# Optimization experiments

Hardware: AMD Instinct MI355X
Metric: run time of the kernel (lower is better)

Reference implementation:

```python
import jax, jax.numpy as jnp
import numpy as np

EPS = 1e-4

def _conv(x, W):
    # x: [B,H,W,Cin], W: [3,3,Cin,Cout] -> SAME submanifold-style dense conv
    return jax.lax.conv_general_dilated(x, W, (1, 1), 'SAME',
                                        dimension_numbers=('NHWC', 'HWIO', 'NHWC'))

def _bn_relu(x, m, g, b):
    # BatchNormReLU over active sites only (scn semantics)
    mm = m[..., None]
    n = jnp.maximum(mm.sum(), 1.0)
    mean = (x * mm).sum((0, 1, 2)) / n
    var = (((x - mean) ** 2) * mm).sum((0, 1, 2)) / n
    y = (x - mean) * jax.lax.rsqrt(var + EPS) * g + b
    return jnp.maximum(y, 0.0) * mm

def _maxpool(x, m):
    # scn.MaxPooling(2, 3, 2): 3x3 window, stride 2, VALID; output active if any input active
    neg = jnp.where(m[..., None] > 0, x, -1e30)
    p = jax.lax.reduce_window(neg, -1e30, jax.lax.max, (1, 3, 3, 1), (1, 2, 2, 1), 'VALID')
    m2 = jax.lax.reduce_window(m, 0.0, jax.lax.max, (1, 3, 3), (1, 2, 2), 'VALID')
    return jnp.where(m2[..., None] > 0, p, 0.0), m2


def setup_inputs() -> dict:
    key = jax.random.key(0)
    ks = jax.random.split(key, 16)
    B, H, W = 2048, 23, 31
    x = jax.random.normal(ks[0], (B, H, W, 2), dtype=jnp.float32)
    mask = jax.random.randint(ks[1], (B, H, W), 0, 2, dtype=jnp.int32)
    def w(k, shape, s=0.05):
        return jax.random.normal(k, shape, dtype=jnp.float32) * s
    params = {
        'x': x, 'mask': mask,
        'W1': w(ks[2], (3, 3, 2, 16)),   'g1': jnp.ones(16),  'b1': jnp.zeros(16),
        'W2': w(ks[3], (3, 3, 16, 32)),  'g2': jnp.ones(32),  'b2': jnp.zeros(32),
        'W3': w(ks[4], (3, 3, 32, 64)),  'g3': jnp.ones(64),  'b3': jnp.zeros(64),
        'W4': w(ks[5], (3, 3, 64, 128)), 'g4': jnp.ones(128), 'b4': jnp.zeros(128),
        'Wl': w(ks[6], (3, 3, 128, 4 * 256)), 'bl': jnp.zeros(4 * 256),
        'lw1': w(ks[7], (8960, 1024), 0.02), 'lb1': jnp.zeros(1024),
        'lw2': w(ks[8], (1024, 5 * 7 * 12), 0.02), 'lb2': jnp.zeros(5 * 7 * 12),
    }
    return params


def reference(x, mask, W1, g1, b1, W2, g2, b2, W3, g3, b3, W4, g4, b4,
              Wl, bl, lw1, lb1, lw2, lb2):
    m = mask.astype(x.dtype)
    xm = x * m[..., None]
    h = _bn_relu(_conv(xm, W1) * m[..., None], m, g1, b1)
    h = _bn_relu(_conv(h, W2) * m[..., None], m, g2, b2)
    h, m = _maxpool(h, m)                          # [B,11,15,32]
    h = _bn_relu(_conv(h, W3) * m[..., None], m, g3, b3)
    h = _bn_relu(_conv(h, W4) * m[..., None], m, g4, b4)
    h, m = _maxpool(h, m)                          # [B,5,7,128]
    # sparse ConvLSTM, single step, zero initial hidden/cell state
    gates = (_conv(h, Wl) + bl) * m[..., None]     # [B,5,7,1024]
    i, f, o, g_ = jnp.split(gates, 4, axis=-1)
    c = jax.nn.sigmoid(i) * jnp.tanh(g_)
    hh = jax.nn.sigmoid(o) * jnp.tanh(c) * m[..., None]  # [B,5,7,256]
    # SparseToDense gives [B,C,H,W]; flatten in (C,H,W) order like torch .view
    flat = jnp.transpose(hh, (0, 3, 1, 2)).reshape(hh.shape[0], -1)  # [B,8960]
    y = jnp.maximum(flat @ lw1 + lb1, 0.0)
    y = y @ lw2 + lb2
    return y.reshape(-1, 5, 7, 12)
```

## Files before the change

### kernel.cpp

```cpp
#include <hip/hip_runtime.h>
#include <hip/hip_bf16.h>
#include <math.h>

using bf16 = __hip_bfloat16;

typedef short s8v __attribute__((ext_vector_type(8)));
typedef float f4v __attribute__((ext_vector_type(4)));

static constexpr int  BB  = 2048;
static constexpr int  IH  = 23, IW = 31;
static constexpr int  PH  = 11, PW = 15;
static constexpr int  QH  = 5,  QW = 7;
static constexpr long NSITE1 = (long)BB * IH * IW;
static constexpr long NSITE2 = (long)BB * PH * PW;
static constexpr long NSITE3 = (long)BB * QH * QW;

static constexpr long OFF_S1 = 0,   OFF_Q1 = 64;
static constexpr long OFF_S2 = 128, OFF_Q2 = 192;
static constexpr long OFF_S3 = 256, OFF_Q3 = 320;
static constexpr long OFF_S4 = 384, OFF_Q4 = 512;
static constexpr long OFF_N1 = 640, OFF_N2 = 641;
static constexpr long OFF_SC1 = 704,  OFF_SH1 = 768;
static constexpr long OFF_SC2 = 832,  OFF_SH2 = 896;
static constexpr long OFF_SC3 = 960,  OFF_SH3 = 1024;
static constexpr long OFF_SC4 = 1088, OFF_SH4 = 1216;
static constexpr long OFF_M0 = 2048;
static constexpr long OFF_M1 = OFF_M0 + NSITE1;
static constexpr long OFF_M2 = OFF_M1 + NSITE2;
static constexpr long OFF_BF = 1871872;
static constexpr long SZ_A   = 43253760L;
static constexpr long WB2_A  = 25000000L;
static constexpr long WB3_B  = 22000000L;
static constexpr long WB4_B  = 22100000L;
static constexpr long WBL_A  = 20000000L;
static constexpr long WFC1_B = 23000000L;
static constexpr long WFC2_B = 33000000L;

__device__ __forceinline__ float b2f(bf16 v) { return __bfloat162float(v); }
__device__ __forceinline__ bf16  f2b(float v) { return __float2bfloat16(v); }
__device__ __forceinline__ float sigmoidf_(float x) {
    return __builtin_amdgcn_rcpf(1.f + __expf(-x));
}
__device__ __forceinline__ float tanhf_(float x) {
    float xc = fminf(fmaxf(x, -15.f), 15.f);
    float t = __expf(-2.f * xc);
    return (1.f - t) * __builtin_amdgcn_rcpf(1.f + t);
}

__device__ __forceinline__ void ld8(const bf16* p, float* f) {
    union { uint4 u; unsigned short s[8]; } cv;
    cv.u = *(const uint4*)p;
#pragma unroll
    for (int i = 0; i < 8; i++) f[i] = __uint_as_float(((unsigned int)cv.s[i]) << 16);
}
__device__ __forceinline__ void st8(bf16* p, const float* f) {
    union { uint4 u; bf16 h[8]; } cv;
#pragma unroll
    for (int i = 0; i < 8; i++) cv.h[i] = f2b(f[i]);
    *(uint4*)p = cv.u;
}

__global__ void cvt_w_k(const float* __restrict__ W, bf16* __restrict__ wb,
                        int CIN, int CINP, int COUT, int total) {
    int idx = blockIdx.x * 256 + threadIdx.x;
    if (idx >= total) return;
    int ci  = idx % CINP;
    int t2  = idx / CINP;
    int co  = t2 % COUT;
    int tap = t2 / COUT;
    wb[idx] = (ci < CIN) ? f2b(W[((long)(tap * CIN + ci)) * COUT + co]) : f2b(0.f);
}

__global__ void cvt_wl3_k(const float* __restrict__ Wl, bf16* __restrict__ wbl3) {
    int idx = blockIdx.x * 256 + threadIdx.x;
    if (idx >= 884736) return;
    int kidx = idx & 31;
    int n    = (idx >> 5) % 768;
    int kk   = (idx >> 5) / 768 % 4;
    int tap  = idx / (32 * 768 * 4);
    int g = n >> 8, c = n & 255;
    int col = (g == 0) ? c : (g == 1 ? 512 + c : 768 + c);
    int cin = kk * 32 + kidx;
    wbl3[idx] = f2b(Wl[((long)(tap * 128 + cin)) * 1024 + col]);
}

__global__ void cvt_fc1T8_k(const float* __restrict__ lw1, bf16* __restrict__ wfc1) {
    int t = blockIdx.x * 256 + threadIdx.x;
    if (t >= 1146880) return;
    int j   = t & 1023;
    int k8g = t >> 10;
    int hw  = k8g >> 5;
    int c8  = k8g & 31;
    float f[8];
#pragma unroll
    for (int c7 = 0; c7 < 8; c7++)
        f[c7] = lw1[((long)((c8 * 8 + c7) * 35 + hw)) * 1024 + j];
    st8(wfc1 + (long)t * 8, f);
}

__global__ void cvt_fc2T8_k(const float* __restrict__ lw2, bf16* __restrict__ whi,
                            bf16* __restrict__ wlo) {
    int t = blockIdx.x * 256 + threadIdx.x;
    if (t >= 57344) return;
    int n  = t % 448;
    int k8 = t / 448;
    union { uint4 u; bf16 h8[8]; } h, l;
#pragma unroll
    for (int ki = 0; ki < 8; ki++) {
        float v = (n < 420) ? lw2[(long)(k8 * 8 + ki) * 420 + n] : 0.f;
        bf16 hb = f2b(v);
        h.h8[ki] = hb;
        l.h8[ki] = f2b(v - b2f(hb));
    }
    *(uint4*)(whi + (long)t * 8) = h.u;
    *(uint4*)(wlo + (long)t * 8) = l.u;
}

__global__ void prep_k(const float* __restrict__ x, const int* __restrict__ mask,
                       float* __restrict__ m0, bf16* __restrict__ xm) {
    long idx = (long)blockIdx.x * 256 + threadIdx.x;
    if (idx >= NSITE1) return;
    float m = (mask[idx] != 0) ? 1.f : 0.f;
    m0[idx] = m;
    xm[idx * 2 + 0] = f2b(x[idx * 2 + 0] * m);
    xm[idx * 2 + 1] = f2b(x[idx * 2 + 1] * m);
}

__global__ void conv1_k(const bf16* __restrict__ xm, const float* __restrict__ Wt,
                        const float* __restrict__ m0, bf16* __restrict__ out) {
    const int H = IH, W = IW;
    long site = (long)blockIdx.x * 256 + threadIdx.x;
    if (site >= NSITE1) return;
    float acc[16];
#pragma unroll
    for (int i = 0; i < 16; i++) acc[i] = 0.f;
    float mk = m0[site];
    if (mk > 0.f) {
        int w = (int)(site % W); int h = (int)((site / W) % H);
        for (int tap = 0; tap < 9; tap++) {
            int dh = tap / 3 - 1, dw = tap % 3 - 1;
            int nh = h + dh, nw = w + dw;
            if (nh < 0 || nh >= H || nw < 0 || nw >= W) continue;
            long ns = site + (long)dh * W + dw;
            float i0 = b2f(xm[ns * 2 + 0]), i1 = b2f(xm[ns * 2 + 1]);
            const float* wp = Wt + tap * 32;
#pragma unroll
            for (int co = 0; co < 16; co++) acc[co] += i0 * wp[co] + i1 * wp[16 + co];
        }
    }
    st8(out + site * 16, acc);
    st8(out + site * 16 + 8, acc + 8);
}

template<int CIN, int CINP, int COUT, int KK, int MT_W, int NT_W, int H, int W, bool ZPAD, bool BN>
__global__ void conv_mfma(const bf16* __restrict__ in, const bf16* __restrict__ wb,
                          const float* __restrict__ mask,
                          const float* __restrict__ scale, const float* __restrict__ shift,
                          bf16* __restrict__ out) {
    constexpr int NT   = COUT / 16;
    constexpr int NWN  = NT / NT_W;
    constexpr int HALO = W + 1;
    constexpr int REG  = 64 + 2 * HALO;
    constexpr int SE   = CIN + 8;
    constexpr int CHPS = CIN / 8;
    __shared__ bf16 smem[(REG + 1) * SE];

    const int tid = threadIdx.x;
    const int wv = tid >> 6;
    const int L  = tid & 63;
    const int q  = (L >> 4);
    const int lm = L & 15;
    const int wn = wv % NWN;
    const int wm = wv / NWN;
    const int mt0 = wm * MT_W;
    const long base = (long)blockIdx.x * 64;
    const long nsites = (long)gridDim.x * 64;

    for (int c = tid; c < REG * CHPS; c += 256) {
        int s = c / CHPS;
        int o = c % CHPS;
        long gs = base - HALO + s;
        uint4 v = {0u, 0u, 0u, 0u};
        if (gs >= 0 && gs < nsites) {
            v = *(const uint4*)(in + gs * CIN + o * 8);
            if (BN) {
                float mk = mask[gs];
                union { uint4 u; unsigned short us[8]; } cv; cv.u = v;
                union { uint4 u; bf16 h[8]; } ov;
#pragma unroll
                for (int i = 0; i < 8; i++) {
                    float f = __uint_as_float(((unsigned int)cv.us[i]) << 16);
                    int ch = o * 8 + i;
                    float r = fmaxf(f * scale[ch] + shift[ch], 0.f);
                    ov.h[i] = f2b(mk > 0.f ? r : 0.f);
                }
                v = ov.u;
            }
        }
        *(uint4*)(smem + s * SE + o * 8) = v;
    }
    if (ZPAD) {
        uint4 z = {0u, 0u, 0u, 0u};
        for (int s = tid; s < REG; s += 256)
            *(uint4*)(smem + s * SE + CIN) = z;
        if (tid == 0)
            *(uint4*)(smem + REG * SE) = z;
    }
    __syncthreads();

    int hh[MT_W], ww[MT_W];
#pragma unroll
    for (int i = 0; i < MT_W; i++) {
        long s = base + (mt0 + i) * 16 + lm;
        ww[i] = (int)(s % W);
        hh[i] = (int)((s / W) % H);
    }
    const int lbase = mt0 * 16 + lm + HALO;

    f4v acc[MT_W][NT_W];
#pragma unroll
    for (int i = 0; i < MT_W; i++)
#pragma unroll
        for (int j = 0; j < NT_W; j++) acc[i][j] = (f4v){0.f, 0.f, 0.f, 0.f};

    for (int tap = 0; tap < 9; tap++) {
        const int dh = tap / 3 - 1, dw = tap % 3 - 1;
        const int dlo = dh * W + dw;
#pragma unroll
        for (int kk = 0; kk < KK; kk++) {
            s8v a[MT_W];
#pragma unroll
            for (int i = 0; i < MT_W; i++) {
                int nh = hh[i] + dh, nw = ww[i] + dw;
                bool ok = (nh >= 0) & (nh < H) & (nw < W) & (nw >= 0);
                s8v t = *(const s8v*)(smem + (lbase + i * 16 + dlo) * SE + kk * 32 + q * 8);
                a[i] = ok ? t : (s8v){0, 0, 0, 0, 0, 0, 0, 0};
            }
#pragma unroll
            for (int j = 0; j < NT_W; j++) {
                int co = (wn * NT_W + j) * 16 + lm;
                s8v b = *(const s8v*)(wb + ((long)(tap * COUT + co)) * CINP + kk * 32 + q * 8);
#pragma unroll
                for (int i = 0; i < MT_W; i++)
                    acc[i][j] = __builtin_amdgcn_mfma_f32_16x16x32_bf16(a[i], b, acc[i][j], 0, 0, 0);
            }
        }
    }
#pragma unroll
    for (int i = 0; i < MT_W; i++) {
#pragma unroll
        for (int r = 0; r < 4; r++) {
            long so = base + (mt0 + i) * 16 + q * 4 + r;
            float mk = mask[so];
#pragma unroll
            for (int j = 0; j < NT_W; j++) {
                int co = (wn * NT_W + j) * 16 + lm;
                out[so * COUT + co] = f2b(mk > 0.f ? acc[i][j][r] : 0.f);
            }
        }
    }
}

template<int C>
__global__ void bn_stats(const bf16* __restrict__ v, const float* __restrict__ mask,
                         float* __restrict__ sum, float* __restrict__ sumsq,
                         float* __restrict__ count, long nsites) {
    __shared__ float s_sum[C], s_ss[C];
    __shared__ float s_cnt;
    int tid = threadIdx.x;
    if (tid < C) { s_sum[tid] = 0.f; s_ss[tid] = 0.f; }
    if (tid == 0) s_cnt = 0.f;
    __syncthreads();
    const long total8 = nsites * C / 8;
    const long stride = (long)gridDim.x * 256;
    const int c0 = (int)((((long)blockIdx.x * 256 + tid) * 8) % C);
    float ls[8], lss[8];
#pragma unroll
    for (int i = 0; i < 8; i++) { ls[i] = 0.f; lss[i] = 0.f; }
    float lc = 0.f;
    for (long e8 = (long)blockIdx.x * 256 + tid; e8 < total8; e8 += stride) {
        long e0 = e8 * 8;
        float f[8];
        ld8(v + e0, f);
#pragma unroll
        for (int i = 0; i < 8; i++) { ls[i] += f[i]; lss[i] += f[i] * f[i]; }
        if (count != nullptr && c0 == 0) lc += (mask[e0 / C] > 0.f) ? 1.f : 0.f;
    }
#pragma unroll
    for (int i = 0; i < 8; i++) {
        atomicAdd(&s_sum[c0 + i], ls[i]);
        atomicAdd(&s_ss[c0 + i], lss[i]);
    }
    if (count != nullptr && c0 == 0) atomicAdd(&s_cnt, lc);
    __syncthreads();
    if (tid < C) { atomicAdd(&sum[tid], s_sum[tid]); atomicAdd(&sumsq[tid], s_ss[tid]); }
    if (count != nullptr && tid == 0) atomicAdd(count, s_cnt);
}

template<int C>
__global__ void bn_param(const float* __restrict__ sum, const float* __restrict__ ss,
                         const float* __restrict__ count,
                         const float* __restrict__ g, const float* __restrict__ b,
                         float* __restrict__ scale, float* __restrict__ shift) {
    int c = threadIdx.x;
    if (c >= C) return;
    float n = fmaxf(count[0], 1.f);
    float mean = sum[c] / n;
    float var  = ss[c] / n - mean * mean;
    float sc = (1.f / sqrtf(var + 1e-4f)) * g[c];
    scale[c] = sc;
    shift[c] = b[c] - mean * sc;
}

template<int C>
__global__ void maxpool_bn(const bf16* __restrict__ in, const float* __restrict__ min_,
                           const float* __restrict__ scale, const float* __restrict__ shift,
                           bf16* __restrict__ out, float* __restrict__ mout,
                           int B, int H, int W, int OH, int OW) {
    long i8 = (long)blockIdx.x * 256 + threadIdx.x;
    long total8 = (long)B * OH * OW * C / 8;
    if (i8 >= total8) return;
    long e0 = i8 * 8;
    int c0 = (int)(e0 % C);
    long osite = e0 / C;
    int ow = (int)(osite % OW); long t2 = osite / OW; int oh = (int)(t2 % OH); long b = t2 / OH;
    float sc[8], sh[8];
#pragma unroll
    for (int i = 0; i < 8; i++) { sc[i] = scale[c0 + i]; sh[i] = shift[c0 + i]; }
    float mm = 0.f, p[8];
#pragma unroll
    for (int i = 0; i < 8; i++) p[i] = -1e30f;
    for (int kh = 0; kh < 3; kh++)
    for (int kw = 0; kw < 3; kw++) {
        int h = oh * 2 + kh, w = ow * 2 + kw;
        long is = ((long)b * H + h) * W + w;
        float mv = min_[is];
        if (mv > 0.f) {
            mm = 1.f;
            float f[8];
            ld8(in + is * C + c0, f);
#pragma unroll
            for (int i = 0; i < 8; i++) p[i] = fmaxf(p[i], f[i] * sc[i] + sh[i]);
        }
    }
    float o[8];
#pragma unroll
    for (int i = 0; i < 8; i++) o[i] = (mm > 0.f) ? fmaxf(p[i], 0.f) : 0.f;
    st8(out + e0, o);
    if (c0 == 0) mout[osite] = mm;
}

__global__ void maxpool_p2t(const bf16* __restrict__ c4, const float* __restrict__ m1,
                            const float* __restrict__ scale, const float* __restrict__ shift,
                            bf16* __restrict__ p2T8, float* __restrict__ m2h) {
    int t = blockIdx.x * 256 + threadIdx.x;
    if (t >= 1146880) return;
    int b  = t & 2047;
    int q2 = t >> 11;
    int hw = q2 % 35;
    int k8 = q2 / 35;
    int oh = hw / QW, ow = hw % QW;
    int c0 = k8 * 8;
    float sc[8], sh[8];
#pragma unroll
    for (int i = 0; i < 8; i++) { sc[i] = scale[c0 + i]; sh[i] = shift[c0 + i]; }
    float mm = 0.f, p[8];
#pragma unroll
    for (int i = 0; i < 8; i++) p[i] = -1e30f;
    for (int kh = 0; kh < 3; kh++)
    for (int kw = 0; kw < 3; kw++) {
        int h = oh * 2 + kh, w = ow * 2 + kw;
        long is = ((long)b * PH + h) * PW + w;
        float mv = m1[is];
        if (mv > 0.f) {
            mm = 1.f;
            float f[8];
            ld8(c4 + is * 128 + c0, f);
#pragma unroll
            for (int i = 0; i < 8; i++) p[i] = fmaxf(p[i], f[i] * sc[i] + sh[i]);
        }
    }
    float o[8];
#pragma unroll
    for (int i = 0; i < 8; i++) o[i] = (mm > 0.f) ? fmaxf(p[i], 0.f) : 0.f;
    st8(p2T8 + (long)t * 8, o);
    if (k8 == 0) m2h[hw * 2048 + b] = mm;
}

__global__ void __launch_bounds__(256, 3)
gates_mfma(const bf16* __restrict__ p2T8, const bf16* __restrict__ wbl3,
           const float* __restrict__ bl, const float* __restrict__ m2h,
           bf16* __restrict__ goutT8) {
    __shared__ bf16 abuf[16 * 64 * 8];
    __shared__ bf16 sm[64][136];
    const int bi = blockIdx.x;
    const int half = bi & 1;
    const int g2 = bi >> 1;
    const int hw = g2 >> 5;
    const int b0 = (g2 & 31) * 64;
    const int h = hw / QW, w = hw % QW;
    const int tid = threadIdx.x;
    const int wv = tid >> 6;
    const int L  = tid & 63;
    const int q  = L >> 4;
    const int lm = L & 15;

    f4v acc[4][2][3];
#pragma unroll
    for (int i = 0; i < 4; i++)
#pragma unroll
        for (int j = 0; j < 2; j++)
#pragma unroll
            for (int g = 0; g < 3; g++) acc[i][j][g] = (f4v){0.f, 0.f, 0.f, 0.f};

    for (int tap = 0; tap < 9; tap++) {
        const int dh = tap / 3 - 1, dw = tap % 3 - 1;
        const int nh = h + dh, nw = w + dw;
        if (nh < 0 || nh >= QH || nw < 0 || nw >= QW) continue;
        const int hwn = hw + dh * QW + dw;

        __syncthreads();
        for (int c = tid; c < 1024; c += 256) {
            int kq = c >> 6;
            int bb = c & 63;
            uint4 v = *(const uint4*)(p2T8 + (((long)(kq * 35 + hwn)) * 2048 + b0 + bb) * 8);
            *(uint4*)(abuf + (long)c * 8) = v;
        }
        __syncthreads();

#pragma unroll
        for (int kk = 0; kk < 4; kk++) {
            s8v a[4];
#pragma unroll
            for (int i = 0; i < 4; i++)
                a[i] = *(const s8v*)(abuf + (((kk * 4 + q) * 64) + i * 16 + lm) * 8);
            const bf16* slab = wbl3 + ((long)(tap * 4 + kk)) * 768 * 32 + (long)q * 8;
#pragma unroll
            for (int j = 0; j < 2; j++) {
                int cc = half * 8 + wv * 2 + j;
#pragma unroll
                for (int g = 0; g < 3; g++) {
                    int n = g * 256 + cc * 16 + lm;
                    s8v b = *(const s8v*)(slab + (long)n * 32);
#pragma unroll
                    for (int i = 0; i < 4; i++)
                        acc[i][j][g] = __builtin_amdgcn_mfma_f32_16x16x32_bf16(a[i], b, acc[i][j][g], 0, 0, 0);
                }
            }
        }
    }
#pragma unroll
    for (int j = 0; j < 2; j++) {
        int cc = half * 8 + wv * 2 + j;
        int c = cc * 16 + lm;
        int cl = (wv * 2 + j) * 16 + lm;
        float bi_ = bl[c], bo_ = bl[512 + c], bg_ = bl[768 + c];
#pragma unroll
        for (int i = 0; i < 4; i++) {
#pragma unroll
            for (int r = 0; r < 4; r++) {
                int b_in = i * 16 + q * 4 + r;
                float m = m2h[hw * 2048 + b0 + b_in];
                float val = 0.f;
                if (m > 0.f) {
                    float iv = acc[i][j][0][r] + bi_;
                    float ov = acc[i][j][1][r] + bo_;
                    float gv = acc[i][j][2][r] + bg_;
                    float ct = sigmoidf_(iv) * tanhf_(gv);
                    val = sigmoidf_(ov) * tanhf_(ct);
                }
                sm[b_in][cl] = f2b(val);
            }
        }
    }
    __syncthreads();
#pragma unroll
    for (int k = 0; k < 4; k++) {
        int e = k * 256 + tid;
        int c8l = e >> 6, b_in = e & 63;
        union { uint4 u; bf16 h8[8]; } v;
#pragma unroll
        for (int i = 0; i < 8; i++) v.h8[i] = sm[b_in][c8l * 8 + i];
        long dst = ((long)(hw * 32 + half * 16 + c8l)) * 2048 + b0 + b_in;
        *(uint4*)(goutT8 + dst * 8) = v.u;
    }
}

__global__ void fc1_mfma(const bf16* __restrict__ AT8, const bf16* __restrict__ WT8,
                         const float* __restrict__ lb1, bf16* __restrict__ y1) {
    const int tid = threadIdx.x;
    const int wv = tid >> 6;
    const int L  = tid & 63;
    const int q  = L >> 4, lm = L & 15;
    const int wm = wv >> 1, wn = wv & 1;
    const int bm = blockIdx.x & 31;
    const int bn = blockIdx.x >> 5;
    const int m0 = bm * 64 + wm * 32;
    const int n0 = bn * 64 + wn * 32;

    f4v acc[2][2];
#pragma unroll
    for (int i = 0; i < 2; i++)
#pragma unroll
        for (int j = 0; j < 2; j++) acc[i][j] = (f4v){0.f, 0.f, 0.f, 0.f};

#pragma unroll 2
    for (int k8 = 0; k8 < 1120; k8 += 4) {
        long ar = ((long)(k8 + q)) * 2048;
        long br = ((long)(k8 + q)) * 1024;
        s8v a0 = *(const s8v*)(AT8 + (ar + m0 + lm) * 8);
        s8v a1 = *(const s8v*)(AT8 + (ar + m0 + 16 + lm) * 8);
        s8v b0 = *(const s8v*)(WT8 + (br + n0 + lm) * 8);
        s8v b1 = *(const s8v*)(WT8 + (br + n0 + 16 + lm) * 8);
        acc[0][0] = __builtin_amdgcn_mfma_f32_16x16x32_bf16(a0, b0, acc[0][0], 0, 0, 0);
        acc[0][1] = __builtin_amdgcn_mfma_f32_16x16x32_bf16(a0, b1, acc[0][1], 0, 0, 0);
        acc[1][0] = __builtin_amdgcn_mfma_f32_16x16x32_bf16(a1, b0, acc[1][0], 0, 0, 0);
        acc[1][1] = __builtin_amdgcn_mfma_f32_16x16x32_bf16(a1, b1, acc[1][1], 0, 0, 0);
    }
#pragma unroll
    for (int i = 0; i < 2; i++) {
#pragma unroll
        for (int j = 0; j < 2; j++) {
            int nn = n0 + j * 16 + lm;
            float bias = lb1[nn];
#pragma unroll
            for (int r = 0; r < 4; r++) {
                int mm = m0 + i * 16 + q * 4 + r;
                y1[(long)mm * 1024 + nn] = f2b(fmaxf(acc[i][j][r] + bias, 0.f));
            }
        }
    }
}

__global__ void fc2_mfma(const bf16* __restrict__ y1, const bf16* __restrict__ whi,
                         const bf16* __restrict__ wlo, const float* __restrict__ lb2,
                         float* __restrict__ out) {
    const int tid = threadIdx.x;
    const int wv = tid >> 6;
    const int L  = tid & 63;
    const int q  = L >> 4, lm = L & 15;
    const int wm = wv >> 1, wn = wv & 1;
    const int bm = blockIdx.x % 32;
    const int bn = blockIdx.x / 32;
    const int m0 = bm * 64 + wm * 32;
    const int n0 = bn * 64 + wn * 32;

    f4v acc[2][2];
#pragma unroll
    for (int i = 0; i < 2; i++)
#pragma unroll
        for (int j = 0; j < 2; j++) acc[i][j] = (f4v){0.f, 0.f, 0.f, 0.f};

#pragma unroll 2
    for (int k8 = 0; k8 < 128; k8 += 4) {
        const bf16* arow = y1 + (long)(k8 + q) * 8;
        long br = ((long)(k8 + q)) * 448;
        s8v a0 = *(const s8v*)(arow + (long)(m0 + lm) * 1024);
        s8v a1 = *(const s8v*)(arow + (long)(m0 + 16 + lm) * 1024);
        s8v h0 = *(const s8v*)(whi + (br + n0 + lm) * 8);
        s8v h1 = *(const s8v*)(whi + (br + n0 + 16 + lm) * 8);
        s8v l0 = *(const s8v*)(wlo + (br + n0 + lm) * 8);
        s8v l1 = *(const s8v*)(wlo + (br + n0 + 16 + lm) * 8);
        acc[0][0] = __builtin_amdgcn_mfma_f32_16x16x32_bf16(a0, h0, acc[0][0], 0, 0, 0);
        acc[0][1] = __builtin_amdgcn_mfma_f32_16x16x32_bf16(a0, h1, acc[0][1], 0, 0, 0);
        acc[1][0] = __builtin_amdgcn_mfma_f32_16x16x32_bf16(a1, h0, acc[1][0], 0, 0, 0);
        acc[1][1] = __builtin_amdgcn_mfma_f32_16x16x32_bf16(a1, h1, acc[1][1], 0, 0, 0);
        acc[0][0] = __builtin_amdgcn_mfma_f32_16x16x32_bf16(a0, l0, acc[0][0], 0, 0, 0);
        acc[0][1] = __builtin_amdgcn_mfma_f32_16x16x32_bf16(a0, l1, acc[0][1], 0, 0, 0);
        acc[1][0] = __builtin_amdgcn_mfma_f32_16x16x32_bf16(a1, l0, acc[1][0], 0, 0, 0);
        acc[1][1] = __builtin_amdgcn_mfma_f32_16x16x32_bf16(a1, l1, acc[1][1], 0, 0, 0);
    }
#pragma unroll
    for (int j = 0; j < 2; j++) {
        int nn = n0 + j * 16 + lm;
        if (nn >= 420) continue;
        float bias = lb2[nn];
#pragma unroll
        for (int i = 0; i < 2; i++) {
#pragma unroll
            for (int r = 0; r < 4; r++) {
                int mm = m0 + i * 16 + q * 4 + r;
                out[(long)mm * 420 + nn] = acc[i][j][r] + bias;
            }
        }
    }
}

extern "C" void kernel_launch(void* const* d_in, const int* in_sizes, int n_in,
                              void* d_out, int out_size, void* d_ws, size_t ws_size,
                              hipStream_t stream) {
    const float* x    = (const float*)d_in[0];
    const int*   mask = (const int*)d_in[1];
    const float* W1 = (const float*)d_in[2];
    const float* g1 = (const float*)d_in[3];
    const float* b1 = (const float*)d_in[4];
    const float* W2 = (const float*)d_in[5];
    const float* g2 = (const float*)d_in[6];
    const float* b2 = (const float*)d_in[7];
    const float* W3 = (const float*)d_in[8];
    const float* g3 = (const float*)d_in[9];
    const float* b3 = (const float*)d_in[10];
    const float* W4 = (const float*)d_in[11];
    const float* g4 = (const float*)d_in[12];
    const float* b4 = (const float*)d_in[13];
    const float* Wl = (const float*)d_in[14];
    const float* bl = (const float*)d_in[15];
    const float* lw1 = (const float*)d_in[16];
    const float* lb1 = (const float*)d_in[17];
    const float* lw2 = (const float*)d_in[18];
    const float* lb2 = (const float*)d_in[19];
    float* out = (float*)d_out;

    float* ws = (float*)d_ws;
    float* m0 = ws + OFF_M0;
    float* m1 = ws + OFF_M1;
    float* m2h = ws + OFF_M2;
    bf16* bufA = (bf16*)(ws + OFF_BF);
    bf16* bufB = bufA + SZ_A;

    bf16* c1     = bufA;
    bf16* xm     = bufB;
    bf16* c2     = bufB;
    bf16* p1     = bufA;
    bf16* c3     = bufB;
    bf16* c4     = bufA;
    bf16* p2T8   = bufB;
    bf16* goutT8 = bufA;
    bf16* y1     = bufB;
    bf16* wb2    = bufA + WB2_A;
    bf16* wb3    = bufB + WB3_B;
    bf16* wb4    = bufB + WB4_B;
    bf16* wbl3   = bufA + WBL_A;
    bf16* wfc1   = bufB + WFC1_B;
    bf16* wfc2h  = bufB + WFC2_B;
    bf16* wfc2l  = wfc2h + 458752;

    hipMemsetAsync(ws, 0, 4096, stream);

    prep_k<<<(int)((NSITE1 + 255) / 256), 256, 0, stream>>>(x, mask, m0, xm);
    cvt_w_k<<<(9216 + 255) / 256, 256, 0, stream>>>(W2, wb2, 16, 32, 32, 9216);

    conv1_k<<<(int)((NSITE1 + 255) / 256), 256, 0, stream>>>(xm, W1, m0, c1);
    bn_stats<16><<<1280, 256, 0, stream>>>(c1, m0, ws + OFF_S1, ws + OFF_Q1, ws + OFF_N1, NSITE1);
    bn_param<16><<<1, 16, 0, stream>>>(ws + OFF_S1, ws + OFF_Q1, ws + OFF_N1, g1, b1, ws + OFF_SC1, ws + OFF_SH1);

    conv_mfma<16, 32, 32, 1, 2, 1, IH, IW, true, true>
        <<<(int)(NSITE1 / 64), 256, 0, stream>>>(c1, wb2, m0, ws + OFF_SC1, ws + OFF_SH1, c2);
    bn_stats<32><<<1280, 256, 0, stream>>>(c2, m0, ws + OFF_S2, ws + OFF_Q2, nullptr, NSITE1);
    bn_param<32><<<1, 32, 0, stream>>>(ws + OFF_S2, ws + OFF_Q2, ws + OFF_N1, g2, b2, ws + OFF_SC2, ws + OFF_SH2);

    maxpool_bn<32><<<(int)(NSITE2 * 32 / 8 / 256), 256, 0, stream>>>(c2, m0, ws + OFF_SC2, ws + OFF_SH2,
                                                                     p1, m1, BB, IH, IW, PH, PW);

    cvt_w_k<<<(18432 + 255) / 256, 256, 0, stream>>>(W3, wb3, 32, 32, 64, 18432);
    cvt_w_k<<<(73728 + 255) / 256, 256, 0, stream>>>(W4, wb4, 64, 64, 128, 73728);
    cvt_fc1T8_k<<<(1146880 + 255) / 256, 256, 0, stream>>>(lw1, wfc1);
    cvt_fc2T8_k<<<(57344 + 255) / 256, 256, 0, stream>>>(lw2, wfc2h, wfc2l);

    conv_mfma<32, 32, 64, 1, 4, 1, PH, PW, false, false>
        <<<(int)(NSITE2 / 64), 256, 0, stream>>>(p1, wb3, m1, ws + OFF_SC2, ws + OFF_SH2, c3);
    bn_stats<64><<<1280, 256, 0, stream>>>(c3, m1, ws + OFF_S3, ws + OFF_Q3, ws + OFF_N2, NSITE2);
    bn_param<64><<<1, 64, 0, stream>>>(ws + OFF_S3, ws + OFF_Q3, ws + OFF_N2, g3, b3, ws + OFF_SC3, ws + OFF_SH3);

    conv_mfma<64, 64, 128, 2, 4, 2, PH, PW, false, true>
        <<<(int)(NSITE2 / 64), 256, 0, stream>>>(c3, wb4, m1, ws + OFF_SC3, ws + OFF_SH3, c4);
    bn_stats<128><<<1280, 256, 0, stream>>>(c4, m1, ws + OFF_S4, ws + OFF_Q4, nullptr, NSITE2);
    bn_param<128><<<1, 128, 0, stream>>>(ws + OFF_S4, ws + OFF_Q4, ws + OFF_N2, g4, b4, ws + OFF_SC4, ws + OFF_SH4);

    maxpool_p2t<<<(1146880 + 255) / 256, 256, 0, stream>>>(c4, m1, ws + OFF_SC4, ws + OFF_SH4, p2T8, m2h);

    cvt_wl3_k<<<(884736 + 255) / 256, 256, 0, stream>>>(Wl, wbl3);

    gates_mfma<<<2240, 256, 0, stream>>>(p2T8, wbl3, bl, m2h, goutT8);

    fc1_mfma<<<512, 256, 0, stream>>>(goutT8, wfc1, lb1, y1);

    fc2_mfma<<<224, 256, 0, stream>>>(y1, wfc2h, wfc2l, lb2, out);
}
```

Before: 926.9 us.

## Fuse BatchNorm statistics into conv epilogues with bucketed global atomics

```diff
diff --git a/kernel.cpp b/kernel.cpp
--- a/kernel.cpp
+++ b/kernel.cpp
@@ -35,6 +35,8 @@
 static constexpr long WBL_A  = 20000000L;
 static constexpr long WFC1_B = 23000000L;
 static constexpr long WFC2_B = 33000000L;
+static constexpr long BKT_A  = 40000000L;
+static constexpr long BKT_B  = 35000000L;
 
 __device__ __forceinline__ float b2f(bf16 v) { return __bfloat162float(v); }
 __device__ __forceinline__ bf16  f2b(float v) { return __float2bfloat16(v); }
@@ -127,36 +129,60 @@
 }
 
 __global__ void conv1_k(const bf16* __restrict__ xm, const float* __restrict__ Wt,
-                        const float* __restrict__ m0, bf16* __restrict__ out) {
+                        const float* __restrict__ m0, bf16* __restrict__ out,
+                        float* __restrict__ bkt, float* __restrict__ cnt) {
+    __shared__ float s_s[16], s_q[16], s_c;
     const int H = IH, W = IW;
-    long site = (long)blockIdx.x * 256 + threadIdx.x;
-    if (site >= NSITE1) return;
+    int tid = threadIdx.x;
+    if (tid < 16) { s_s[tid] = 0.f; s_q[tid] = 0.f; }
+    if (tid == 0) s_c = 0.f;
+    __syncthreads();
+    long site = (long)blockIdx.x * 256 + tid;
     float acc[16];
 #pragma unroll
     for (int i = 0; i < 16; i++) acc[i] = 0.f;
-    float mk = m0[site];
-    if (mk > 0.f) {
-        int w = (int)(site % W); int h = (int)((site / W) % H);
-        for (int tap = 0; tap < 9; tap++) {
-            int dh = tap / 3 - 1, dw = tap % 3 - 1;
-            int nh = h + dh, nw = w + dw;
-            if (nh < 0 || nh >= H || nw < 0 || nw >= W) continue;
-            long ns = site + (long)dh * W + dw;
-            float i0 = b2f(xm[ns * 2 + 0]), i1 = b2f(xm[ns * 2 + 1]);
-            const float* wp = Wt + tap * 32;
-#pragma unroll
-            for (int co = 0; co < 16; co++) acc[co] += i0 * wp[co] + i1 * wp[16 + co];
-        }
-    }
-    st8(out + site * 16, acc);
-    st8(out + site * 16 + 8, acc + 8);
-}
-
-template<int CIN, int CINP, int COUT, int KK, int MT_W, int NT_W, int H, int W, bool ZPAD, bool BN>
+    float mk = 0.f;
+    if (site < NSITE1) {
+        mk = m0[site];
+        if (mk > 0.f) {
+            int w = (int)(site % W); int h = (int)((site / W) % H);
+            for (int tap = 0; tap < 9; tap++) {
+                int dh = tap / 3 - 1, dw = tap % 3 - 1;
+                int nh = h + dh, nw = w + dw;
+                if (nh < 0 || nh >= H || nw < 0 || nw >= W) continue;
+                long ns = site + (long)dh * W + dw;
+                float i0 = b2f(xm[ns * 2 + 0]), i1 = b2f(xm[ns * 2 + 1]);
+                const float* wp = Wt + tap * 32;
+#pragma unroll
+                for (int co = 0; co < 16; co++) acc[co] += i0 * wp[co] + i1 * wp[16 + co];
+            }
+        }
+        st8(out + site * 16, acc);
+        st8(out + site * 16 + 8, acc + 8);
+#pragma unroll
+        for (int i = 0; i < 16; i++) {
+            float vb = b2f(f2b(acc[i]));
+            atomicAdd(&s_s[i], vb);
+            atomicAdd(&s_q[i], vb * vb);
+        }
+        if (mk > 0.f) atomicAdd(&s_c, 1.f);
+    }
+    __syncthreads();
+    int bk = blockIdx.x & 63;
+    if (tid < 16) {
+        atomicAdd(bkt + (long)bk * 32 + tid, s_s[tid]);
+        atomicAdd(bkt + (long)bk * 32 + 16 + tid, s_q[tid]);
+    }
+    if (tid == 0) atomicAdd(cnt, s_c);
+}
+
+template<int CIN, int CINP, int COUT, int KK, int MT_W, int NT_W, int H, int W,
+         bool ZPAD, bool BN, bool STATS, bool CNT>
 __global__ void conv_mfma(const bf16* __restrict__ in, const bf16* __restrict__ wb,
                           const float* __restrict__ mask,
                           const float* __restrict__ scale, const float* __restrict__ shift,
-                          bf16* __restrict__ out) {
+                          bf16* __restrict__ out,
+                          float* __restrict__ bkt, float* __restrict__ cnt) {
     constexpr int NT   = COUT / 16;
     constexpr int NWN  = NT / NT_W;
     constexpr int HALO = W + 1;
@@ -164,6 +190,7 @@
     constexpr int SE   = CIN + 8;
     constexpr int CHPS = CIN / 8;
     __shared__ bf16 smem[(REG + 1) * SE];
+    __shared__ float s_s[COUT], s_q[COUT], s_c;
 
     const int tid = threadIdx.x;
     const int wv = tid >> 6;
@@ -206,6 +233,10 @@
         if (tid == 0)
             *(uint4*)(smem + REG * SE) = z;
     }
+    if (STATS) {
+        if (tid < COUT) { s_s[tid] = 0.f; s_q[tid] = 0.f; }
+        if (tid == 0) s_c = 0.f;
+    }
     __syncthreads();
 
     int hh[MT_W], ww[MT_W];
@@ -246,67 +277,59 @@
             }
         }
     }
+
+    float ls[NT_W], lq[NT_W];
+#pragma unroll
+    for (int j = 0; j < NT_W; j++) { ls[j] = 0.f; lq[j] = 0.f; }
+    float lc = 0.f;
 #pragma unroll
     for (int i = 0; i < MT_W; i++) {
 #pragma unroll
         for (int r = 0; r < 4; r++) {
             long so = base + (mt0 + i) * 16 + q * 4 + r;
             float mk = mask[so];
+            if (CNT) { if (wv == 0 && lm == 0) lc += (mk > 0.f) ? 1.f : 0.f; }
 #pragma unroll
             for (int j = 0; j < NT_W; j++) {
                 int co = (wn * NT_W + j) * 16 + lm;
-                out[so * COUT + co] = f2b(mk > 0.f ? acc[i][j][r] : 0.f);
-            }
-        }
+                bf16 ob = f2b(mk > 0.f ? acc[i][j][r] : 0.f);
+                out[so * COUT + co] = ob;
+                if (STATS) { float vb = b2f(ob); ls[j] += vb; lq[j] += vb * vb; }
+            }
+        }
+    }
+    if (STATS) {
+#pragma unroll
+        for (int j = 0; j < NT_W; j++) {
+            int co = (wn * NT_W + j) * 16 + lm;
+            atomicAdd(&s_s[co], ls[j]);
+            atomicAdd(&s_q[co], lq[j]);
+        }
+        if (CNT && wv == 0 && lm == 0) atomicAdd(&s_c, lc);
+        __syncthreads();
+        int bk = blockIdx.x & 63;
+        if (tid < COUT) {
+            atomicAdd(bkt + (long)bk * 2 * COUT + tid, s_s[tid]);
+            atomicAdd(bkt + (long)bk * 2 * COUT + COUT + tid, s_q[tid]);
+        }
+        if (CNT && tid == 0) atomicAdd(cnt, s_c);
     }
 }
 
 template<int C>
-__global__ void bn_stats(const bf16* __restrict__ v, const float* __restrict__ mask,
-                         float* __restrict__ sum, float* __restrict__ sumsq,
-                         float* __restrict__ count, long nsites) {
-    __shared__ float s_sum[C], s_ss[C];
-    __shared__ float s_cnt;
-    int tid = threadIdx.x;
-    if (tid < C) { s_sum[tid] = 0.f; s_ss[tid] = 0.f; }
-    if (tid == 0) s_cnt = 0.f;
-    __syncthreads();
-    const long total8 = nsites * C / 8;
-    const long stride = (long)gridDim.x * 256;
-    const int c0 = (int)((((long)blockIdx.x * 256 + tid) * 8) % C);
-    float ls[8], lss[8];
-#pragma unroll
-    for (int i = 0; i < 8; i++) { ls[i] = 0.f; lss[i] = 0.f; }
-    float lc = 0.f;
-    for (long e8 = (long)blockIdx.x * 256 + tid; e8 < total8; e8 += stride) {
-        long e0 = e8 * 8;
-        float f[8];
-        ld8(v + e0, f);
-#pragma unroll
-        for (int i = 0; i < 8; i++) { ls[i] += f[i]; lss[i] += f[i] * f[i]; }
-        if (count != nullptr && c0 == 0) lc += (mask[e0 / C] > 0.f) ? 1.f : 0.f;
-    }
-#pragma unroll
-    for (int i = 0; i < 8; i++) {
-        atomicAdd(&s_sum[c0 + i], ls[i]);
-        atomicAdd(&s_ss[c0 + i], lss[i]);
-    }
-    if (count != nullptr && c0 == 0) atomicAdd(&s_cnt, lc);
-    __syncthreads();
-    if (tid < C) { atomicAdd(&sum[tid], s_sum[tid]); atomicAdd(&sumsq[tid], s_ss[tid]); }
-    if (count != nullptr && tid == 0) atomicAdd(count, s_cnt);
-}
-
-template<int C>
-__global__ void bn_param(const float* __restrict__ sum, const float* __restrict__ ss,
-                         const float* __restrict__ count,
-                         const float* __restrict__ g, const float* __restrict__ b,
-                         float* __restrict__ scale, float* __restrict__ shift) {
+__global__ void bn_param_bkt(const float* __restrict__ bkt, const float* __restrict__ count,
+                             const float* __restrict__ g, const float* __restrict__ b,
+                             float* __restrict__ scale, float* __restrict__ shift) {
     int c = threadIdx.x;
     if (c >= C) return;
+    float s = 0.f, q2 = 0.f;
+    for (int k = 0; k < 64; k++) {
+        s  += bkt[(long)k * 2 * C + c];
+        q2 += bkt[(long)k * 2 * C + C + c];
+    }
     float n = fmaxf(count[0], 1.f);
-    float mean = sum[c] / n;
-    float var  = ss[c] / n - mean * mean;
+    float mean = s / n;
+    float var  = q2 / n - mean * mean;
     float sc = (1.f / sqrtf(var + 1e-4f)) * g[c];
     scale[c] = sc;
     shift[c] = b[c] - mean * sc;
@@ -635,37 +658,43 @@
     bf16* wfc2h  = bufB + WFC2_B;
     bf16* wfc2l  = wfc2h + 458752;
 
+    float* bkt16  = (float*)(bufA + BKT_A);
+    float* bkt32  = bkt16 + 2048;
+    float* bkt64  = bkt32 + 4096;
+    float* bkt128 = (float*)(bufB + BKT_B);
+
     hipMemsetAsync(ws, 0, 4096, stream);
+    hipMemsetAsync(bkt16, 0, (2048 + 4096 + 8192) * 4, stream);
 
     prep_k<<<(int)((NSITE1 + 255) / 256), 256, 0, stream>>>(x, mask, m0, xm);
     cvt_w_k<<<(9216 + 255) / 256, 256, 0, stream>>>(W2, wb2, 16, 32, 32, 9216);
 
-    conv1_k<<<(int)((NSITE1 + 255) / 256), 256, 0, stream>>>(xm, W1, m0, c1);
-    bn_stats<16><<<1280, 256, 0, stream>>>(c1, m0, ws + OFF_S1, ws + OFF_Q1, ws + OFF_N1, NSITE1);
-    bn_param<16><<<1, 16, 0, stream>>>(ws + OFF_S1, ws + OFF_Q1, ws + OFF_N1, g1, b1, ws + OFF_SC1, ws + OFF_SH1);
-
-    conv_mfma<16, 32, 32, 1, 2, 1, IH, IW, true, true>
-        <<<(int)(NSITE1 / 64), 256, 0, stream>>>(c1, wb2, m0, ws + OFF_SC1, ws + OFF_SH1, c2);
-    bn_stats<32><<<1280, 256, 0, stream>>>(c2, m0, ws + OFF_S2, ws + OFF_Q2, nullptr, NSITE1);
-    bn_param<32><<<1, 32, 0, stream>>>(ws + OFF_S2, ws + OFF_Q2, ws + OFF_N1, g2, b2, ws + OFF_SC2, ws + OFF_SH2);
+    conv1_k<<<(int)((NSITE1 + 255) / 256), 256, 0, stream>>>(xm, W1, m0, c1, bkt16, ws + OFF_N1);
+    bn_param_bkt<16><<<1, 16, 0, stream>>>(bkt16, ws + OFF_N1, g1, b1, ws + OFF_SC1, ws + OFF_SH1);
+
+    conv_mfma<16, 32, 32, 1, 2, 1, IH, IW, true, true, true, false>
+        <<<(int)(NSITE1 / 64), 256, 0, stream>>>(c1, wb2, m0, ws + OFF_SC1, ws + OFF_SH1, c2,
+                                                 bkt32, nullptr);
+    bn_param_bkt<32><<<1, 32, 0, stream>>>(bkt32, ws + OFF_N1, g2, b2, ws + OFF_SC2, ws + OFF_SH2);
 
     maxpool_bn<32><<<(int)(NSITE2 * 32 / 8 / 256), 256, 0, stream>>>(c2, m0, ws + OFF_SC2, ws + OFF_SH2,
                                                                      p1, m1, BB, IH, IW, PH, PW);
 
+    hipMemsetAsync(bkt128, 0, 16384 * 4, stream);
     cvt_w_k<<<(18432 + 255) / 256, 256, 0, stream>>>(W3, wb3, 32, 32, 64, 18432);
     cvt_w_k<<<(73728 + 255) / 256, 256, 0, stream>>>(W4, wb4, 64, 64, 128, 73728);
     cvt_fc1T8_k<<<(1146880 + 255) / 256, 256, 0, stream>>>(lw1, wfc1);
     cvt_fc2T8_k<<<(57344 + 255) / 256, 256, 0, stream>>>(lw2, wfc2h, wfc2l);
 
-    conv_mfma<32, 32, 64, 1, 4, 1, PH, PW, false, false>
-        <<<(int)(NSITE2 / 64), 256, 0, stream>>>(p1, wb3, m1, ws + OFF_SC2, ws + OFF_SH2, c3);
-    bn_stats<64><<<1280, 256, 0, stream>>>(c3, m1, ws + OFF_S3, ws + OFF_Q3, ws + OFF_N2, NSITE2);
-    bn_param<64><<<1, 64, 0, stream>>>(ws + OFF_S3, ws + OFF_Q3, ws + OFF_N2, g3, b3, ws + OFF_SC3, ws + OFF_SH3);
-
-    conv_mfma<64, 64, 128, 2, 4, 2, PH, PW, false, true>
-        <<<(int)(NSITE2 / 64), 256, 0, stream>>>(c3, wb4, m1, ws + OFF_SC3, ws + OFF_SH3, c4);
-    bn_stats<128><<<1280, 256, 0, stream>>>(c4, m1, ws + OFF_S4, ws + OFF_Q4, nullptr, NSITE2);
-    bn_param<128><<<1, 128, 0, stream>>>(ws + OFF_S4, ws + OFF_Q4, ws + OFF_N2, g4, b4, ws + OFF_SC4, ws + OFF_SH4);
+    conv_mfma<32, 32, 64, 1, 4, 1, PH, PW, false, false, true, true>
+        <<<(int)(NSITE2 / 64), 256, 0, stream>>>(p1, wb3, m1, ws + OFF_SC2, ws + OFF_SH2, c3,
+                                                 bkt64, ws + OFF_N2);
+    bn_param_bkt<64><<<1, 64, 0, stream>>>(bkt64, ws + OFF_N2, g3, b3, ws + OFF_SC3, ws + OFF_SH3);
+
+    conv_mfma<64, 64, 128, 2, 4, 2, PH, PW, false, true, true, false>
+        <<<(int)(NSITE2 / 64), 256, 0, stream>>>(c3, wb4, m1, ws + OFF_SC3, ws + OFF_SH3, c4,
+                                                 bkt128, nullptr);
+    bn_param_bkt<128><<<1, 128, 0, stream>>>(bkt128, ws + OFF_N2, g4, b4, ws + OFF_SC4, ws + OFF_SH4);
 
     maxpool_p2t<<<(1146880 + 255) / 256, 256, 0, stream>>>(c4, m1, ws + OFF_SC4, ws + OFF_SH4, p2T8, m2h);
 
```

New measurement: 1.196 ms. 1.29x slower.
